# Kernel optimization log

Measured on AMD Instinct MI355X. Metric: run time of the kernel, lower is better.

## Reference

```python
import jax, jax.numpy as jnp
import numpy as np

LOSS_WEIGHT = 1.0


def setup_inputs() -> dict:
    key = jax.random.key(0)
    k1, k2 = jax.random.split(key)
    source = jax.random.normal(k1, (8, 4096, 3), dtype=jnp.float32)
    target = jax.random.normal(k2, (8, 4096, 3), dtype=jnp.float32)
    return {"source": source, "target": target}


def reference(source, target):
    # Pairwise Euclidean distances via the Gram-matrix identity (same math as torch.cdist):
    # d(i,j)^2 = ||s_i||^2 + ||t_j||^2 - 2 <s_i, t_j>
    s2 = jnp.sum(source * source, axis=-1)  # [B, N]
    t2 = jnp.sum(target * target, axis=-1)  # [B, M]
    cross = jnp.einsum("bnd,bmd->bnm", source, target)  # [B, N, M]
    d2 = s2[:, :, None] + t2[:, None, :] - 2.0 * cross
    dists = jnp.sqrt(jnp.maximum(d2, 0.0))  # [B, N, M]
    term1 = jnp.mean(jnp.min(dists, axis=2), axis=1)  # source -> nearest target
    term2 = jnp.mean(jnp.min(dists, axis=1), axis=1)  # target -> nearest source
    return LOSS_WEIGHT * (jnp.mean(term1) + jnp.mean(term2))
```

## Files before the change

kernel.cpp:

```cpp
#include <hip/hip_runtime.h>

#define BB 8
#define NN 4096
#define NPTS (2*BB*NN)
#define PARTIAL_OFF (1 << 20)
#define RPT 4
#define ROWS 256
#define WVS 16
#define JSL (NN/WVS)

__global__ __launch_bounds__(256) void cd_pack(const float* __restrict__ src,
                                               const float* __restrict__ tgt,
                                               float4* __restrict__ pk) {
    int i = blockIdx.x * 256 + threadIdx.x;
    const float* p = ((i >> 15) ? tgt : src) + 3 * (i & 32767);
    float x = p[0], y = p[1], z = p[2];
    pk[i] = make_float4(x, y, z, 0.5f * (x*x + y*y + z*z));
}

__global__ __launch_bounds__(1024) void cd_scan(const float4* __restrict__ pk,
                                                float* __restrict__ partial) {
    __shared__ float pm[WVS][ROWS];
    __shared__ float bs[WVS];
    const int dir = blockIdx.z;
    const int b   = blockIdx.y;
    const int rt  = blockIdx.x;
    const int tid = threadIdx.x, lane = tid & 63, wave = tid >> 6;

    const float4* S = pk + (dir ? (size_t)BB*NN : 0) + (size_t)b*NN;
    const float4* T = pk + (dir ? 0 : (size_t)BB*NN) + (size_t)b*NN;

    float nx[RPT], ny[RPT], nz[RPT], q[RPT];
#pragma unroll
    for (int r = 0; r < RPT; ++r) {
        float4 s = S[rt*ROWS + r*64 + lane];
        nx[r] = -s.x; ny[r] = -s.y; nz[r] = -s.z; q[r] = s.w;
    }

    const int jbase = __builtin_amdgcn_readfirstlane(wave * JSL);
    const float4* Tw = T + jbase;

    float m[RPT];
#pragma unroll
    for (int r = 0; r < RPT; ++r) m[r] = 1.0e30f;

    for (int j = 0; j < JSL; j += 8) {
        float4 t0 = Tw[j],   t1 = Tw[j+1], t2 = Tw[j+2], t3 = Tw[j+3];
        float4 t4 = Tw[j+4], t5 = Tw[j+5], t6 = Tw[j+6], t7 = Tw[j+7];
#pragma unroll
        for (int r = 0; r < RPT; ++r) {
            float a0 = fmaf(nx[r], t0.x, fmaf(ny[r], t0.y, fmaf(nz[r], t0.z, t0.w)));
            float a1 = fmaf(nx[r], t1.x, fmaf(ny[r], t1.y, fmaf(nz[r], t1.z, t1.w)));
            float a2 = fmaf(nx[r], t2.x, fmaf(ny[r], t2.y, fmaf(nz[r], t2.z, t2.w)));
            float a3 = fmaf(nx[r], t3.x, fmaf(ny[r], t3.y, fmaf(nz[r], t3.z, t3.w)));
            float a4 = fmaf(nx[r], t4.x, fmaf(ny[r], t4.y, fmaf(nz[r], t4.z, t4.w)));
            float a5 = fmaf(nx[r], t5.x, fmaf(ny[r], t5.y, fmaf(nz[r], t5.z, t5.w)));
            float a6 = fmaf(nx[r], t6.x, fmaf(ny[r], t6.y, fmaf(nz[r], t6.z, t6.w)));
            float a7 = fmaf(nx[r], t7.x, fmaf(ny[r], t7.y, fmaf(nz[r], t7.z, t7.w)));
            float b0 = fminf(a0, a1), b1 = fminf(a2, a3);
            float b2 = fminf(a4, a5), b3 = fminf(a6, a7);
            m[r] = fminf(m[r], fminf(fminf(b0, b1), fminf(b2, b3)));
        }
    }

#pragma unroll
    for (int r = 0; r < RPT; ++r)
        pm[wave][r*64 + lane] = m[r] + q[r];
    __syncthreads();

    float d = 0.0f;
    if (tid < ROWS) {
        float v = pm[0][tid];
#pragma unroll
        for (int s = 1; s < WVS; ++s) v = fminf(v, pm[s][tid]);
        v = fmaxf(v, 0.0f);
        d = sqrtf(2.0f * v);
    }
#pragma unroll
    for (int o = 32; o > 0; o >>= 1) d += __shfl_down(d, o, 64);
    if (lane == 0) bs[wave] = d;
    __syncthreads();
    if (tid == 0) {
        float t = 0.0f;
#pragma unroll
        for (int w = 0; w < WVS; ++w) t += bs[w];
        partial[((size_t)dir*BB + b)*16 + rt] = t;
    }
}

__global__ __launch_bounds__(256) void cd_final(const float* __restrict__ partial,
                                                float* __restrict__ out) {
    __shared__ float ps[4];
    float v = partial[threadIdx.x];
#pragma unroll
    for (int o = 32; o > 0; o >>= 1) v += __shfl_down(v, o, 64);
    if ((threadIdx.x & 63) == 0) ps[threadIdx.x >> 6] = v;
    __syncthreads();
    if (threadIdx.x == 0) {
        out[0] = (ps[0] + ps[1] + ps[2] + ps[3]) * (1.0f / (float)(BB * NN));
    }
}

extern "C" void kernel_launch(void* const* d_in, const int* in_sizes, int n_in,
                              void* d_out, int out_size, void* d_ws, size_t ws_size,
                              hipStream_t stream) {
    const float* src = (const float*)d_in[0];
    const float* tgt = (const float*)d_in[1];
    float4* pk = (float4*)d_ws;
    float* partial = (float*)((char*)d_ws + PARTIAL_OFF);
    float* out = (float*)d_out;

    cd_pack<<<NPTS / 256, 256, 0, stream>>>(src, tgt, pk);
    dim3 grid(NN / ROWS, BB, 2);
    cd_scan<<<grid, 1024, 0, stream>>>(pk, partial);
    cd_final<<<1, 256, 0, stream>>>(partial, out);
}
```

Before: 90.17 us.

## Stage target chunks in LDS, double rows per thread, split j-range across blocks

The scan kernel now loads a half-range chunk of packed target points into shared memory and reads them from LDS instead of global memory. Each thread handles 8 rows instead of 4, and the target range is split into two chunks processed by separate blocks, keeping the grid at 256 blocks. Per-row minima from both chunks are written to a global buffer. A single 1024-thread final kernel combines them and does the sqrt and sum. This increases register pressure and moves 65536 sqrt/min operations into a one-block final kernel, which may serialize.

```diff
diff --git a/kernel.cpp b/kernel.cpp
--- a/kernel.cpp
+++ b/kernel.cpp
@@ -3,11 +3,14 @@
 #define BB 8
 #define NN 4096
 #define NPTS (2*BB*NN)
-#define PARTIAL_OFF (1 << 20)
-#define RPT 4
-#define ROWS 256
+#define GMIN_OFF (1 << 20)
+#define RPT 8
+#define ROWS 512
 #define WVS 16
-#define JSL (NN/WVS)
+#define JC 2
+#define JCHUNK (NN/JC)
+#define JSL (JCHUNK/WVS)
+#define TOTROWS (2*BB*NN)
 
 __global__ __launch_bounds__(256) void cd_pack(const float* __restrict__ src,
                                                const float* __restrict__ tgt,
@@ -19,16 +22,20 @@
 }
 
 __global__ __launch_bounds__(1024) void cd_scan(const float4* __restrict__ pk,
-                                                float* __restrict__ partial) {
+                                                float* __restrict__ gmin) {
+    __shared__ float4 tl[JCHUNK];
     __shared__ float pm[WVS][ROWS];
-    __shared__ float bs[WVS];
     const int dir = blockIdx.z;
     const int b   = blockIdx.y;
-    const int rt  = blockIdx.x;
+    const int rt  = blockIdx.x >> 1;
+    const int jc  = blockIdx.x & 1;
     const int tid = threadIdx.x, lane = tid & 63, wave = tid >> 6;
 
     const float4* S = pk + (dir ? (size_t)BB*NN : 0) + (size_t)b*NN;
-    const float4* T = pk + (dir ? 0 : (size_t)BB*NN) + (size_t)b*NN;
+    const float4* T = pk + (dir ? 0 : (size_t)BB*NN) + (size_t)b*NN + (size_t)jc*JCHUNK;
+
+    tl[tid]        = T[tid];
+    tl[tid + 1024] = T[tid + 1024];
 
     float nx[RPT], ny[RPT], nz[RPT], q[RPT];
 #pragma unroll
@@ -36,30 +43,25 @@
         float4 s = S[rt*ROWS + r*64 + lane];
         nx[r] = -s.x; ny[r] = -s.y; nz[r] = -s.z; q[r] = s.w;
     }
+    __syncthreads();
 
-    const int jbase = __builtin_amdgcn_readfirstlane(wave * JSL);
-    const float4* Tw = T + jbase;
-
+    const int jofs = wave * JSL;
     float m[RPT];
 #pragma unroll
     for (int r = 0; r < RPT; ++r) m[r] = 1.0e30f;
 
-    for (int j = 0; j < JSL; j += 8) {
-        float4 t0 = Tw[j],   t1 = Tw[j+1], t2 = Tw[j+2], t3 = Tw[j+3];
-        float4 t4 = Tw[j+4], t5 = Tw[j+5], t6 = Tw[j+6], t7 = Tw[j+7];
+    for (int j = 0; j < JSL; j += 4) {
+        float4 t0 = tl[jofs + j];
+        float4 t1 = tl[jofs + j + 1];
+        float4 t2 = tl[jofs + j + 2];
+        float4 t3 = tl[jofs + j + 3];
 #pragma unroll
         for (int r = 0; r < RPT; ++r) {
             float a0 = fmaf(nx[r], t0.x, fmaf(ny[r], t0.y, fmaf(nz[r], t0.z, t0.w)));
             float a1 = fmaf(nx[r], t1.x, fmaf(ny[r], t1.y, fmaf(nz[r], t1.z, t1.w)));
             float a2 = fmaf(nx[r], t2.x, fmaf(ny[r], t2.y, fmaf(nz[r], t2.z, t2.w)));
             float a3 = fmaf(nx[r], t3.x, fmaf(ny[r], t3.y, fmaf(nz[r], t3.z, t3.w)));
-            float a4 = fmaf(nx[r], t4.x, fmaf(ny[r], t4.y, fmaf(nz[r], t4.z, t4.w)));
-            float a5 = fmaf(nx[r], t5.x, fmaf(ny[r], t5.y, fmaf(nz[r], t5.z, t5.w)));
-            float a6 = fmaf(nx[r], t6.x, fmaf(ny[r], t6.y, fmaf(nz[r], t6.z, t6.w)));
-            float a7 = fmaf(nx[r], t7.x, fmaf(ny[r], t7.y, fmaf(nz[r], t7.z, t7.w)));
-            float b0 = fminf(a0, a1), b1 = fminf(a2, a3);
-            float b2 = fminf(a4, a5), b3 = fminf(a6, a7);
-            m[r] = fminf(m[r], fminf(fminf(b0, b1), fminf(b2, b3)));
+            m[r] = fminf(m[r], fminf(fminf(a0, a1), fminf(a2, a3)));
         }
     }
 
@@ -68,36 +70,32 @@
         pm[wave][r*64 + lane] = m[r] + q[r];
     __syncthreads();
 
-    float d = 0.0f;
     if (tid < ROWS) {
         float v = pm[0][tid];
 #pragma unroll
         for (int s = 1; s < WVS; ++s) v = fminf(v, pm[s][tid]);
-        v = fmaxf(v, 0.0f);
-        d = sqrtf(2.0f * v);
-    }
-#pragma unroll
-    for (int o = 32; o > 0; o >>= 1) d += __shfl_down(d, o, 64);
-    if (lane == 0) bs[wave] = d;
-    __syncthreads();
-    if (tid == 0) {
-        float t = 0.0f;
-#pragma unroll
-        for (int w = 0; w < WVS; ++w) t += bs[w];
-        partial[((size_t)dir*BB + b)*16 + rt] = t;
+        gmin[(size_t)jc*TOTROWS + ((size_t)dir*BB + b)*NN + rt*ROWS + tid] = v;
     }
 }
 
-__global__ __launch_bounds__(256) void cd_final(const float* __restrict__ partial,
-                                                float* __restrict__ out) {
-    __shared__ float ps[4];
-    float v = partial[threadIdx.x];
+__global__ __launch_bounds__(1024) void cd_final(const float* __restrict__ gmin,
+                                                 float* __restrict__ out) {
+    __shared__ float ps[16];
+    float sum = 0.0f;
+    for (int i = threadIdx.x; i < TOTROWS; i += 1024) {
+        float v = fminf(gmin[i], gmin[TOTROWS + i]);
+        v = fmaxf(v, 0.0f);
+        sum += sqrtf(2.0f * v);
+    }
 #pragma unroll
-    for (int o = 32; o > 0; o >>= 1) v += __shfl_down(v, o, 64);
-    if ((threadIdx.x & 63) == 0) ps[threadIdx.x >> 6] = v;
+    for (int o = 32; o > 0; o >>= 1) sum += __shfl_down(sum, o, 64);
+    if ((threadIdx.x & 63) == 0) ps[threadIdx.x >> 6] = sum;
     __syncthreads();
     if (threadIdx.x == 0) {
-        out[0] = (ps[0] + ps[1] + ps[2] + ps[3]) * (1.0f / (float)(BB * NN));
+        float t = 0.0f;
+#pragma unroll
+        for (int w = 0; w < 16; ++w) t += ps[w];
+        out[0] = t * (1.0f / (float)(BB * NN));
     }
 }
 
@@ -107,11 +105,11 @@
     const float* src = (const float*)d_in[0];
     const float* tgt = (const float*)d_in[1];
     float4* pk = (float4*)d_ws;
-    float* partial = (float*)((char*)d_ws + PARTIAL_OFF);
+    float* gmin = (float*)((char*)d_ws + GMIN_OFF);
     float* out = (float*)d_out;
 
     cd_pack<<<NPTS / 256, 256, 0, stream>>>(src, tgt, pk);
-    dim3 grid(NN / ROWS, BB, 2);
-    cd_scan<<<grid, 1024, 0, stream>>>(pk, partial);
-    cd_final<<<1, 256, 0, stream>>>(partial, out);
+    dim3 grid((NN / ROWS) * JC, BB, 2);
+    cd_scan<<<grid, 1024, 0, stream>>>(pk, gmin);
+    cd_final<<<1, 1024, 0, stream>>>(gmin, out);
 }
```

After: 102.9 us. 14.1% more time.
